# Kernel optimization log

Hardware: AMD Instinct MI355X
Metric: run time of the kernel (lower is better)

Reference implementation:

```python
import jax, jax.numpy as jnp
import numpy as np

B, N, D = 4, 1024, 1024      # batch, seq_len, query_dim
H, DH = 16, 64               # heads, dim_head; inner = H*DH = 1024
INNER = H * DH
SCALE = DH ** -0.5


def setup_inputs() -> dict:
    key = jax.random.key(0)
    ks = jax.random.split(key, 8)
    x = jax.random.normal(ks[0], (B, N, D), dtype=jnp.float32)
    rel_pos = jax.random.normal(ks[1], (B * H, N, N), dtype=jnp.float32)
    query_mask = jax.random.randint(ks[2], (B, N), 0, 2).astype(bool)
    context_mask = jax.random.randint(ks[3], (B, N), 0, 2).astype(bool)
    # Linear weights stored (in, out); to_q/to_kv have no bias, to_out has bias.
    Wq = jax.random.normal(ks[4], (D, INNER), dtype=jnp.float32) / np.sqrt(D)
    Wkv = jax.random.normal(ks[5], (D, 2 * INNER), dtype=jnp.float32) / np.sqrt(D)
    Wo = jax.random.normal(ks[6], (INNER, D), dtype=jnp.float32) / np.sqrt(INNER)
    bo = jax.random.normal(ks[7], (D,), dtype=jnp.float32) * 0.01
    return {"x": x, "rel_pos": rel_pos, "query_mask": query_mask,
            "context_mask": context_mask, "Wq": Wq, "Wkv": Wkv, "Wo": Wo, "bo": bo}


def reference(x, rel_pos, query_mask, context_mask, Wq, Wkv, Wo, bo):
    # Self-attention (context = x)
    q = x @ Wq                                 # [B, N, INNER]
    kv = x @ Wkv                               # [B, N, 2*INNER]
    k, v = jnp.split(kv, 2, axis=-1)
    # (b n (h d)) -> (b h n d)
    split_heads = lambda t: t.reshape(B, N, H, DH).transpose(0, 2, 1, 3)
    q, k, v = map(split_heads, (q, k, v))
    sim = jnp.einsum('bhid,bhjd->bhij', q, k) * SCALE
    sim = sim + rel_pos.reshape(B, H, N, N)
    neg = -jnp.finfo(sim.dtype).max
    # query_mask: (b i) -> mask rows; context_mask: (b j) -> mask cols
    sim = jnp.where(query_mask[:, None, :, None], sim, neg)
    sim = jnp.where(context_mask[:, None, None, :], sim, neg)
    attn = jax.nn.softmax(sim, axis=-1)
    out = jnp.einsum('bhij,bhjd->bhid', attn, v)    # [B, H, N, DH]
    out = out.transpose(0, 2, 1, 3).reshape(B, N, INNER)
    return out @ Wo + bo
```

## Files before the change

kernel.cpp:

```cpp
#include <hip/hip_runtime.h>


#define NEGMAX 3.402823466e+38f

typedef short short8 __attribute__((ext_vector_type(8)));
typedef float f32x4 __attribute__((ext_vector_type(4)));

__device__ __forceinline__ unsigned short f2bf(float f) {
  unsigned int u = __float_as_uint(f);
  u += 0x7FFFu + ((u >> 16) & 1u);
  return (unsigned short)(u >> 16);
}

__global__ void cast_x_k(const float* __restrict__ x, unsigned short* __restrict__ xb) {
  int i = (blockIdx.x * 256 + threadIdx.x) * 4;
  float4 v = *(const float4*)(x + i);
  ushort4 o;
  o.x = f2bf(v.x); o.y = f2bf(v.y); o.z = f2bf(v.z); o.w = f2bf(v.w);
  *(ushort4*)(xb + i) = o;
}

__global__ void cast_w3t_k(const float* __restrict__ Wq, const float* __restrict__ Wkv,
                           unsigned short* __restrict__ w3t) {
  int t = blockIdx.x * 256 + threadIdx.x;
  int n = t >> 8;
  int d0 = (t & 255) * 4;
  for (int j = 0; j < 4; ++j) {
    int d = d0 + j;
    float v = (n < 1024) ? Wq[(size_t)d * 1024 + n]
                         : Wkv[(size_t)d * 2048 + (n - 1024)];
    w3t[(size_t)n * 1024 + d] = f2bf(v);
  }
}

__global__ void cast_wot_k(const float* __restrict__ Wo, unsigned short* __restrict__ wot) {
  int t = blockIdx.x * 256 + threadIdx.x;
  int n = t >> 8;
  int d0 = (t & 255) * 4;
  for (int j = 0; j < 4; ++j) {
    int d = d0 + j;
    wot[(size_t)n * 1024 + d] = f2bf(Wo[(size_t)d * 1024 + n]);
  }
}

template <int MODE>
__global__ __launch_bounds__(256) void gemm_bt_k(
    const unsigned short* __restrict__ A, const unsigned short* __restrict__ Bt,
    unsigned short* __restrict__ qws, unsigned short* __restrict__ kws,
    unsigned short* __restrict__ vtws,
    const float* __restrict__ bias, float* __restrict__ Cout) {
  constexpr int K = 1024;
  constexpr int NKB = K / 32;
  __shared__ alignas(16) unsigned short As[128 * 32];
  __shared__ alignas(16) unsigned short Bs[128 * 32];
  const int tid = threadIdx.x;
  const int lane = tid & 63, w = tid >> 6;
  const int quad = lane >> 4, lanelo = lane & 15;
  const int tRow = blockIdx.y * 128, tCol = blockIdx.x * 128;
  const int wr = (w >> 1) * 64, wc = (w & 1) * 64;
  const char* AgB = (const char*)(A + (size_t)tRow * K);
  const char* BgB = (const char*)(Bt + (size_t)tCol * K);
  const int c0 = tid, c1 = tid + 256;
  const size_t a0off = (size_t)(c0 >> 2) * 2048 + (c0 & 3) * 16;
  const size_t a1off = (size_t)(c1 >> 2) * 2048 + (c1 & 3) * 16;

  f32x4 acc[4][4];
#pragma unroll
  for (int i = 0; i < 4; ++i)
#pragma unroll
    for (int j = 0; j < 4; ++j) acc[i][j] = (f32x4){0.f, 0.f, 0.f, 0.f};

  int4 ra0 = *(const int4*)(AgB + a0off);
  int4 ra1 = *(const int4*)(AgB + a1off);
  int4 rb0 = *(const int4*)(BgB + a0off);
  int4 rb1 = *(const int4*)(BgB + a1off);

  for (int kb = 0; kb < NKB; ++kb) {
    __syncthreads();
    *(int4*)((char*)As + c0 * 16) = ra0;
    *(int4*)((char*)As + c1 * 16) = ra1;
    *(int4*)((char*)Bs + c0 * 16) = rb0;
    *(int4*)((char*)Bs + c1 * 16) = rb1;
    __syncthreads();
    if (kb + 1 < NKB) {
      const size_t ko = (size_t)(kb + 1) * 64;
      ra0 = *(const int4*)(AgB + a0off + ko);
      ra1 = *(const int4*)(AgB + a1off + ko);
      rb0 = *(const int4*)(BgB + a0off + ko);
      rb1 = *(const int4*)(BgB + a1off + ko);
    }
    short8 af[4], bf[4];
#pragma unroll
    for (int i = 0; i < 4; ++i)
      af[i] = *(const short8*)(As + (wr + i * 16 + lanelo) * 32 + quad * 8);
#pragma unroll
    for (int j = 0; j < 4; ++j)
      bf[j] = *(const short8*)(Bs + (wc + j * 16 + lanelo) * 32 + quad * 8);
#pragma unroll
    for (int i = 0; i < 4; ++i)
#pragma unroll
      for (int j = 0; j < 4; ++j)
        acc[i][j] = __builtin_amdgcn_mfma_f32_16x16x32_bf16(af[i], bf[j], acc[i][j], 0, 0, 0);
  }

  if (MODE == 0) {
#pragma unroll
    for (int i = 0; i < 4; ++i) {
      int row = tRow + wr + i * 16 + quad * 4;
      int b_ = row >> 10;
      int npos = row & 1023;
#pragma unroll
      for (int j = 0; j < 4; ++j) {
        int col = tCol + wc + j * 16 + lanelo;
        if (col < 2048) {
          unsigned short* dst = (col < 1024) ? qws : kws;
          int c = col & 1023;
          int hh = c >> 6, dh = c & 63;
          size_t base = ((size_t)(b_ * 16 + hh) * 1024 + npos) * 64 + dh;
#pragma unroll
          for (int r = 0; r < 4; ++r) dst[base + (size_t)r * 64] = f2bf(acc[i][j][r]);
        } else {
          int c = col - 2048;
          ushort4 pk;
          pk.x = f2bf(acc[i][j][0]);
          pk.y = f2bf(acc[i][j][1]);
          pk.z = f2bf(acc[i][j][2]);
          pk.w = f2bf(acc[i][j][3]);
          *(ushort4*)&vtws[((size_t)(b_ * 16 + (c >> 6)) * 64 + (c & 63)) * 1024 + npos] = pk;
        }
      }
    }
  } else {
#pragma unroll
    for (int i = 0; i < 4; ++i) {
      int row = tRow + wr + i * 16 + quad * 4;
#pragma unroll
      for (int j = 0; j < 4; ++j) {
        int col = tCol + wc + j * 16 + lanelo;
        float bv = bias[col];
#pragma unroll
        for (int r = 0; r < 4; ++r)
          Cout[(size_t)(row + r) * 1024 + col] = acc[i][j][r] + bv;
      }
    }
  }
}

__global__ __launch_bounds__(256) void attn_k(
    const unsigned short* __restrict__ q_ws, const unsigned short* __restrict__ k_ws,
    const unsigned short* __restrict__ vt_ws, const float* __restrict__ rel,
    const int* __restrict__ qmask, const int* __restrict__ cmask,
    unsigned short* __restrict__ aout) {
  constexpr float SCALE = 0.125f;
  __shared__ alignas(16) unsigned short Kl[32 * 72];
  __shared__ alignas(16) unsigned short Vl[64 * 40];
  __shared__ alignas(16) unsigned short Pl[4 * 16 * 40];
  __shared__ float cml[1024];

  const int tid = threadIdx.x;
  const int w = tid >> 6, lane = tid & 63;
  const int quad = lane >> 4, lanelo = lane & 15;
  const int bh = blockIdx.y, b_ = bh >> 4, h = bh & 15;
  const int qrow0 = blockIdx.x * 64 + w * 16;

  for (int i = tid; i < 1024; i += 256)
    cml[i] = (cmask[b_ * 1024 + i] != 0) ? 1.f : 0.f;

  const unsigned short* qg = q_ws + ((size_t)bh * 1024 + qrow0) * 64;
  short8 qf0 = *(const short8*)(qg + (size_t)lanelo * 64 + quad * 8);
  short8 qf1 = *(const short8*)(qg + (size_t)lanelo * 64 + 32 + quad * 8);

  float qmv[4];
#pragma unroll
  for (int r = 0; r < 4; ++r)
    qmv[r] = (qmask[b_ * 1024 + qrow0 + quad * 4 + r] != 0) ? 1.f : 0.f;

  f32x4 o[4];
#pragma unroll
  for (int g = 0; g < 4; ++g) o[g] = (f32x4){0.f, 0.f, 0.f, 0.f};
  float m_run[4], l_run[4];
#pragma unroll
  for (int r = 0; r < 4; ++r) { m_run[r] = -NEGMAX; l_run[r] = 0.f; }

  const char* kgB = (const char*)(k_ws + (size_t)bh * 65536);
  const char* vgB = (const char*)(vt_ws + (size_t)bh * 65536);
  const float* relg = rel + ((size_t)bh * 1024 + qrow0) * 1024;
  unsigned short* pw = Pl + w * 640;

  int4 kc = *(const int4*)(kgB + (size_t)(tid >> 3) * 128 + (tid & 7) * 16);
  int4 vc = *(const int4*)(vgB + (size_t)(tid >> 2) * 2048 + (tid & 3) * 16);

  for (int kb = 0; kb < 32; ++kb) {
    __syncthreads();
    *(int4*)((char*)Kl + (tid >> 3) * 144 + (tid & 7) * 16) = kc;
    *(int4*)((char*)Vl + (tid >> 2) * 80 + (tid & 3) * 16) = vc;
    __syncthreads();
    if (kb + 1 < 32) {
      kc = *(const int4*)(kgB + (size_t)((kb + 1) * 32 + (tid >> 3)) * 128 + (tid & 7) * 16);
      vc = *(const int4*)(vgB + (size_t)(tid >> 2) * 2048 + (size_t)(kb + 1) * 64 + (tid & 3) * 16);
    }

    f32x4 s0 = (f32x4){0.f, 0.f, 0.f, 0.f}, s1 = s0;
    {
      short8 kf;
      kf = *(const short8*)((const char*)Kl + lanelo * 144 + quad * 16);
      s0 = __builtin_amdgcn_mfma_f32_16x16x32_bf16(qf0, kf, s0, 0, 0, 0);
      kf = *(const short8*)((const char*)Kl + lanelo * 144 + 64 + quad * 16);
      s0 = __builtin_amdgcn_mfma_f32_16x16x32_bf16(qf1, kf, s0, 0, 0, 0);
      kf = *(const short8*)((const char*)Kl + (16 + lanelo) * 144 + quad * 16);
      s1 = __builtin_amdgcn_mfma_f32_16x16x32_bf16(qf0, kf, s1, 0, 0, 0);
      kf = *(const short8*)((const char*)Kl + (16 + lanelo) * 144 + 64 + quad * 16);
      s1 = __builtin_amdgcn_mfma_f32_16x16x32_bf16(qf1, kf, s1, 0, 0, 0);
    }

    const int key0 = kb * 32 + lanelo;
    const float cm0 = cml[key0 & 1023], cm1 = cml[(key0 + 16) & 1023];
    float sv[2][4];
#pragma unroll
    for (int r = 0; r < 4; ++r) {
      const float* rrow = relg + (size_t)(quad * 4 + r) * 1024;
      float x0 = s0[r] * SCALE + rrow[key0];
      float x1 = s1[r] * SCALE + rrow[key0 + 16];
      bool qok = qmv[r] != 0.f;
      sv[0][r] = (qok && cm0 != 0.f) ? x0 : -NEGMAX;
      sv[1][r] = (qok && cm1 != 0.f) ? x1 : -NEGMAX;
    }

#pragma unroll
    for (int r = 0; r < 4; ++r) {
      float mloc = fmaxf(sv[0][r], sv[1][r]);
      for (int off = 1; off < 16; off <<= 1) mloc = fmaxf(mloc, __shfl_xor(mloc, off));
      float mnew = fmaxf(m_run[r], mloc);
      float alpha = __expf(m_run[r] - mnew);
      m_run[r] = mnew;
      float p0 = __expf(sv[0][r] - mnew);
      float p1 = __expf(sv[1][r] - mnew);
      float ps = p0 + p1;
      for (int off = 1; off < 16; off <<= 1) ps += __shfl_xor(ps, off);
      l_run[r] = l_run[r] * alpha + ps;
#pragma unroll
      for (int g = 0; g < 4; ++g) o[g][r] *= alpha;
      pw[(quad * 4 + r) * 40 + lanelo] = f2bf(p0);
      pw[(quad * 4 + r) * 40 + 16 + lanelo] = f2bf(p1);
    }

    short8 pa = *(const short8*)(pw + lanelo * 40 + quad * 8);
#pragma unroll
    for (int g = 0; g < 4; ++g) {
      short8 vb = *(const short8*)((const char*)Vl + (g * 16 + lanelo) * 80 + quad * 16);
      o[g] = __builtin_amdgcn_mfma_f32_16x16x32_bf16(pa, vb, o[g], 0, 0, 0);
    }
  }

#pragma unroll
  for (int r = 0; r < 4; ++r) {
    float inv = 1.f / l_run[r];
    size_t row = (size_t)(b_ * 1024 + qrow0 + quad * 4 + r) * 1024;
#pragma unroll
    for (int g = 0; g < 4; ++g)
      aout[row + h * 64 + g * 16 + lanelo] = f2bf(o[g][r] * inv);
  }
}

extern "C" void kernel_launch(void* const* d_in, const int* in_sizes, int n_in,
                              void* d_out, int out_size, void* d_ws, size_t ws_size,
                              hipStream_t stream) {
  const float* x = (const float*)d_in[0];
  const float* rel = (const float*)d_in[1];
  const int* qmask = (const int*)d_in[2];
  const int* cmask = (const int*)d_in[3];
  const float* Wq = (const float*)d_in[4];
  const float* Wkv = (const float*)d_in[5];
  const float* Wo = (const float*)d_in[6];
  const float* bo = (const float*)d_in[7];
  float* out = (float*)d_out;

  char* ws = (char*)d_ws;
  const size_t MB = 1024 * 1024;
  unsigned short* w3t = (unsigned short*)(ws);
  unsigned short* wot = (unsigned short*)(ws + 6 * MB);
  unsigned short* xb  = (unsigned short*)(ws + 8 * MB);
  unsigned short* qws = (unsigned short*)(ws + 16 * MB);
  unsigned short* kws = (unsigned short*)(ws + 24 * MB);
  unsigned short* vtws = (unsigned short*)(ws + 32 * MB);
  unsigned short* aout = xb;

  cast_x_k<<<4096, 256, 0, stream>>>(x, xb);
  cast_w3t_k<<<3072, 256, 0, stream>>>(Wq, Wkv, w3t);
  cast_wot_k<<<1024, 256, 0, stream>>>(Wo, wot);
  gemm_bt_k<0><<<dim3(24, 32), 256, 0, stream>>>(xb, w3t, qws, kws, vtws, nullptr, nullptr);
  attn_k<<<dim3(16, 64), 256, 0, stream>>>(qws, kws, vtws, rel, qmask, cmask, aout);
  gemm_bt_k<1><<<dim3(8, 32), 256, 0, stream>>>(aout, wot, nullptr, nullptr, nullptr, bo, out);
}
```

Baseline: 552.9 us.

## Tile weight transposes via LDS, use direct global-to-LDS loads, widen attention key blocks

The weight cast kernels are replaced by a single LDS-tiled transpose-and-cast kernel, so both reads and writes are coalesced instead of strided. The GEMM now stages A and B tiles straight into LDS with global_load_lds (when the builtin is available) instead of going through registers. That path gives up the old register prefetch, so loads for the next tile no longer overlap compute. The attention kernel moves from 32-key to 64-key blocks, halving barrier and online-softmax rescale steps, and prefetches the next rel_pos tile into registers, at the cost of more registers and LDS.

```diff
diff --git a/kernel.cpp b/kernel.cpp
--- a/kernel.cpp
+++ b/kernel.cpp
@@ -10,6 +10,16 @@
   unsigned int u = __float_as_uint(f);
   u += 0x7FFFu + ((u >> 16) & 1u);
   return (unsigned short)(u >> 16);
+}
+
+__device__ __forceinline__ void stage16(const void* g, void* lds_base, int lane) {
+#if __has_builtin(__builtin_amdgcn_global_load_lds)
+  __builtin_amdgcn_global_load_lds(
+      (const __attribute__((address_space(1))) unsigned int*)g,
+      (__attribute__((address_space(3))) unsigned int*)lds_base, 16, 0, 0);
+#else
+  *(int4*)((char*)lds_base + lane * 16) = *(const int4*)g;
+#endif
 }
 
 __global__ void cast_x_k(const float* __restrict__ x, unsigned short* __restrict__ xb) {
@@ -20,26 +30,21 @@
   *(ushort4*)(xb + i) = o;
 }
 
-__global__ void cast_w3t_k(const float* __restrict__ Wq, const float* __restrict__ Wkv,
-                           unsigned short* __restrict__ w3t) {
-  int t = blockIdx.x * 256 + threadIdx.x;
-  int n = t >> 8;
-  int d0 = (t & 255) * 4;
-  for (int j = 0; j < 4; ++j) {
-    int d = d0 + j;
-    float v = (n < 1024) ? Wq[(size_t)d * 1024 + n]
-                         : Wkv[(size_t)d * 2048 + (n - 1024)];
-    w3t[(size_t)n * 1024 + d] = f2bf(v);
-  }
-}
-
-__global__ void cast_wot_k(const float* __restrict__ Wo, unsigned short* __restrict__ wot) {
-  int t = blockIdx.x * 256 + threadIdx.x;
-  int n = t >> 8;
-  int d0 = (t & 255) * 4;
-  for (int j = 0; j < 4; ++j) {
-    int d = d0 + j;
-    wot[(size_t)n * 1024 + d] = f2bf(Wo[(size_t)d * 1024 + n]);
+__global__ __launch_bounds__(256) void tcast_k(const float* __restrict__ src, int ldsrc,
+                                               unsigned short* __restrict__ dst) {
+  __shared__ float T[64][65];
+  const int n0 = blockIdx.x * 64, d0 = blockIdx.y * 64;
+  const int tx = threadIdx.x & 63, ty = threadIdx.x >> 6;
+#pragma unroll
+  for (int k = 0; k < 16; ++k) {
+    int dl = k * 4 + ty;
+    T[dl][tx] = src[(size_t)(d0 + dl) * ldsrc + n0 + tx];
+  }
+  __syncthreads();
+#pragma unroll
+  for (int k = 0; k < 16; ++k) {
+    int nl = k * 4 + ty;
+    dst[(size_t)(n0 + nl) * 1024 + d0 + tx] = f2bf(T[tx][nl]);
   }
 }
 
@@ -63,6 +68,10 @@
   const int c0 = tid, c1 = tid + 256;
   const size_t a0off = (size_t)(c0 >> 2) * 2048 + (c0 & 3) * 16;
   const size_t a1off = (size_t)(c1 >> 2) * 2048 + (c1 & 3) * 16;
+  char* ldsA0 = (char*)As + w * 1024;
+  char* ldsA1 = (char*)As + 4096 + w * 1024;
+  char* ldsB0 = (char*)Bs + w * 1024;
+  char* ldsB1 = (char*)Bs + 4096 + w * 1024;
 
   f32x4 acc[4][4];
 #pragma unroll
@@ -70,25 +79,15 @@
 #pragma unroll
     for (int j = 0; j < 4; ++j) acc[i][j] = (f32x4){0.f, 0.f, 0.f, 0.f};
 
-  int4 ra0 = *(const int4*)(AgB + a0off);
-  int4 ra1 = *(const int4*)(AgB + a1off);
-  int4 rb0 = *(const int4*)(BgB + a0off);
-  int4 rb1 = *(const int4*)(BgB + a1off);
-
   for (int kb = 0; kb < NKB; ++kb) {
+    if (kb) __syncthreads();
+    const size_t ko = (size_t)kb * 64;
+    stage16(AgB + a0off + ko, ldsA0, lane);
+    stage16(AgB + a1off + ko, ldsA1, lane);
+    stage16(BgB + a0off + ko, ldsB0, lane);
+    stage16(BgB + a1off + ko, ldsB1, lane);
     __syncthreads();
-    *(int4*)((char*)As + c0 * 16) = ra0;
-    *(int4*)((char*)As + c1 * 16) = ra1;
-    *(int4*)((char*)Bs + c0 * 16) = rb0;
-    *(int4*)((char*)Bs + c1 * 16) = rb1;
-    __syncthreads();
-    if (kb + 1 < NKB) {
-      const size_t ko = (size_t)(kb + 1) * 64;
-      ra0 = *(const int4*)(AgB + a0off + ko);
-      ra1 = *(const int4*)(AgB + a1off + ko);
-      rb0 = *(const int4*)(BgB + a0off + ko);
-      rb1 = *(const int4*)(BgB + a1off + ko);
-    }
+
     short8 af[4], bf[4];
 #pragma unroll
     for (int i = 0; i < 4; ++i)
@@ -152,9 +151,9 @@
     const int* __restrict__ qmask, const int* __restrict__ cmask,
     unsigned short* __restrict__ aout) {
   constexpr float SCALE = 0.125f;
-  __shared__ alignas(16) unsigned short Kl[32 * 72];
-  __shared__ alignas(16) unsigned short Vl[64 * 40];
-  __shared__ alignas(16) unsigned short Pl[4 * 16 * 40];
+  __shared__ alignas(16) unsigned short Kl[64 * 72];
+  __shared__ alignas(16) unsigned short Vl[64 * 72];
+  __shared__ alignas(16) unsigned short Pl[4 * 16 * 72];
   __shared__ float cml[1024];
 
   const int tid = threadIdx.x;
@@ -185,70 +184,103 @@
   const char* kgB = (const char*)(k_ws + (size_t)bh * 65536);
   const char* vgB = (const char*)(vt_ws + (size_t)bh * 65536);
   const float* relg = rel + ((size_t)bh * 1024 + qrow0) * 1024;
-  unsigned short* pw = Pl + w * 640;
-
-  int4 kc = *(const int4*)(kgB + (size_t)(tid >> 3) * 128 + (tid & 7) * 16);
-  int4 vc = *(const int4*)(vgB + (size_t)(tid >> 2) * 2048 + (tid & 3) * 16);
-
-  for (int kb = 0; kb < 32; ++kb) {
+  unsigned short* pw = Pl + w * 16 * 72;
+
+  const int k0 = tid >> 3, ch0 = tid & 7;
+  int4 kc0 = *(const int4*)(kgB + (size_t)k0 * 128 + ch0 * 16);
+  int4 kc1 = *(const int4*)(kgB + (size_t)(k0 + 32) * 128 + ch0 * 16);
+  int4 vc0 = *(const int4*)(vgB + (size_t)k0 * 2048 + ch0 * 16);
+  int4 vc1 = *(const int4*)(vgB + (size_t)(k0 + 32) * 2048 + ch0 * 16);
+
+  float rl[4][4];
+#pragma unroll
+  for (int r = 0; r < 4; ++r)
+#pragma unroll
+    for (int c = 0; c < 4; ++c)
+      rl[r][c] = relg[(size_t)(quad * 4 + r) * 1024 + c * 16 + lanelo];
+
+  for (int kb = 0; kb < 16; ++kb) {
     __syncthreads();
-    *(int4*)((char*)Kl + (tid >> 3) * 144 + (tid & 7) * 16) = kc;
-    *(int4*)((char*)Vl + (tid >> 2) * 80 + (tid & 3) * 16) = vc;
+    *(int4*)((char*)Kl + k0 * 144 + ch0 * 16) = kc0;
+    *(int4*)((char*)Kl + (k0 + 32) * 144 + ch0 * 16) = kc1;
+    *(int4*)((char*)Vl + k0 * 144 + ch0 * 16) = vc0;
+    *(int4*)((char*)Vl + (k0 + 32) * 144 + ch0 * 16) = vc1;
     __syncthreads();
-    if (kb + 1 < 32) {
-      kc = *(const int4*)(kgB + (size_t)((kb + 1) * 32 + (tid >> 3)) * 128 + (tid & 7) * 16);
-      vc = *(const int4*)(vgB + (size_t)(tid >> 2) * 2048 + (size_t)(kb + 1) * 64 + (tid & 3) * 16);
-    }
-
-    f32x4 s0 = (f32x4){0.f, 0.f, 0.f, 0.f}, s1 = s0;
-    {
-      short8 kf;
-      kf = *(const short8*)((const char*)Kl + lanelo * 144 + quad * 16);
-      s0 = __builtin_amdgcn_mfma_f32_16x16x32_bf16(qf0, kf, s0, 0, 0, 0);
-      kf = *(const short8*)((const char*)Kl + lanelo * 144 + 64 + quad * 16);
-      s0 = __builtin_amdgcn_mfma_f32_16x16x32_bf16(qf1, kf, s0, 0, 0, 0);
-      kf = *(const short8*)((const char*)Kl + (16 + lanelo) * 144 + quad * 16);
-      s1 = __builtin_amdgcn_mfma_f32_16x16x32_bf16(qf0, kf, s1, 0, 0, 0);
-      kf = *(const short8*)((const char*)Kl + (16 + lanelo) * 144 + 64 + quad * 16);
-      s1 = __builtin_amdgcn_mfma_f32_16x16x32_bf16(qf1, kf, s1, 0, 0, 0);
-    }
-
-    const int key0 = kb * 32 + lanelo;
-    const float cm0 = cml[key0 & 1023], cm1 = cml[(key0 + 16) & 1023];
-    float sv[2][4];
+    if (kb + 1 < 16) {
+      const size_t kof = (size_t)(kb + 1) * 64;
+      kc0 = *(const int4*)(kgB + (kof + k0) * 128 + ch0 * 16);
+      kc1 = *(const int4*)(kgB + (kof + k0 + 32) * 128 + ch0 * 16);
+      vc0 = *(const int4*)(vgB + (size_t)k0 * 2048 + kof * 2 + ch0 * 16);
+      vc1 = *(const int4*)(vgB + (size_t)(k0 + 32) * 2048 + kof * 2 + ch0 * 16);
+    }
+
+    f32x4 s[4];
+#pragma unroll
+    for (int c = 0; c < 4; ++c) {
+      s[c] = (f32x4){0.f, 0.f, 0.f, 0.f};
+      short8 kfa = *(const short8*)((const char*)Kl + (c * 16 + lanelo) * 144 + quad * 16);
+      s[c] = __builtin_amdgcn_mfma_f32_16x16x32_bf16(qf0, kfa, s[c], 0, 0, 0);
+      short8 kfb = *(const short8*)((const char*)Kl + (c * 16 + lanelo) * 144 + 64 + quad * 16);
+      s[c] = __builtin_amdgcn_mfma_f32_16x16x32_bf16(qf1, kfb, s[c], 0, 0, 0);
+    }
+
+    float rln[4][4];
+    if (kb + 1 < 16) {
+#pragma unroll
+      for (int r = 0; r < 4; ++r)
+#pragma unroll
+        for (int c = 0; c < 4; ++c)
+          rln[r][c] = relg[(size_t)(quad * 4 + r) * 1024 + (kb + 1) * 64 + c * 16 + lanelo];
+    }
+
+    float cm[4];
+#pragma unroll
+    for (int c = 0; c < 4; ++c) cm[c] = cml[kb * 64 + c * 16 + lanelo];
+
 #pragma unroll
     for (int r = 0; r < 4; ++r) {
-      const float* rrow = relg + (size_t)(quad * 4 + r) * 1024;
-      float x0 = s0[r] * SCALE + rrow[key0];
-      float x1 = s1[r] * SCALE + rrow[key0 + 16];
-      bool qok = qmv[r] != 0.f;
-      sv[0][r] = (qok && cm0 != 0.f) ? x0 : -NEGMAX;
-      sv[1][r] = (qok && cm1 != 0.f) ? x1 : -NEGMAX;
-    }
-
-#pragma unroll
-    for (int r = 0; r < 4; ++r) {
-      float mloc = fmaxf(sv[0][r], sv[1][r]);
+      const bool qok = qmv[r] != 0.f;
+      float x[4], mloc = -NEGMAX;
+#pragma unroll
+      for (int c = 0; c < 4; ++c) {
+        x[c] = (qok && cm[c] != 0.f) ? s[c][r] * SCALE + rl[r][c] : -NEGMAX;
+        mloc = fmaxf(mloc, x[c]);
+      }
       for (int off = 1; off < 16; off <<= 1) mloc = fmaxf(mloc, __shfl_xor(mloc, off));
       float mnew = fmaxf(m_run[r], mloc);
       float alpha = __expf(m_run[r] - mnew);
       m_run[r] = mnew;
-      float p0 = __expf(sv[0][r] - mnew);
-      float p1 = __expf(sv[1][r] - mnew);
-      float ps = p0 + p1;
+      float ps = 0.f;
+      unsigned short pb[4];
+#pragma unroll
+      for (int c = 0; c < 4; ++c) {
+        float p = __expf(x[c] - mnew);
+        ps += p;
+        pb[c] = f2bf(p);
+      }
       for (int off = 1; off < 16; off <<= 1) ps += __shfl_xor(ps, off);
       l_run[r] = l_run[r] * alpha + ps;
 #pragma unroll
       for (int g = 0; g < 4; ++g) o[g][r] *= alpha;
-      pw[(quad * 4 + r) * 40 + lanelo] = f2bf(p0);
-      pw[(quad * 4 + r) * 40 + 16 + lanelo] = f2bf(p1);
-    }
-
-    short8 pa = *(const short8*)(pw + lanelo * 40 + quad * 8);
-#pragma unroll
-    for (int g = 0; g < 4; ++g) {
-      short8 vb = *(const short8*)((const char*)Vl + (g * 16 + lanelo) * 80 + quad * 16);
-      o[g] = __builtin_amdgcn_mfma_f32_16x16x32_bf16(pa, vb, o[g], 0, 0, 0);
+#pragma unroll
+      for (int c = 0; c < 4; ++c) pw[(quad * 4 + r) * 72 + c * 16 + lanelo] = pb[c];
+    }
+
+    if (kb + 1 < 16) {
+#pragma unroll
+      for (int r = 0; r < 4; ++r)
+#pragma unroll
+        for (int c = 0; c < 4; ++c) rl[r][c] = rln[r][c];
+    }
+
+#pragma unroll
+    for (int c2 = 0; c2 < 2; ++c2) {
+      short8 pa = *(const short8*)((const char*)pw + lanelo * 144 + c2 * 64 + quad * 16);
+#pragma unroll
+      for (int g = 0; g < 4; ++g) {
+        short8 vb = *(const short8*)((const char*)Vl + (g * 16 + lanelo) * 144 + c2 * 64 + quad * 16);
+        o[g] = __builtin_amdgcn_mfma_f32_16x16x32_bf16(pa, vb, o[g], 0, 0, 0);
+      }
     }
   }
 
@@ -286,8 +318,9 @@
   unsigned short* aout = xb;
 
   cast_x_k<<<4096, 256, 0, stream>>>(x, xb);
-  cast_w3t_k<<<3072, 256, 0, stream>>>(Wq, Wkv, w3t);
-  cast_wot_k<<<1024, 256, 0, stream>>>(Wo, wot);
+  tcast_k<<<dim3(16, 16), 256, 0, stream>>>(Wq, 1024, w3t);
+  tcast_k<<<dim3(32, 16), 256, 0, stream>>>(Wkv, 2048, w3t + (size_t)1024 * 1024);
+  tcast_k<<<dim3(16, 16), 256, 0, stream>>>(Wo, 1024, wot);
   gemm_bt_k<0><<<dim3(24, 32), 256, 0, stream>>>(xb, w3t, qws, kws, vtws, nullptr, nullptr);
   attn_k<<<dim3(16, 64), 256, 0, stream>>>(qws, kws, vtws, rel, qmask, cmask, aout);
   gemm_bt_k<1><<<dim3(8, 32), 256, 0, stream>>>(aout, wot, nullptr, nullptr, nullptr, bo, out);
```

New measurement: 493.9 us. -10.7%, faster.
